# Kernel optimization log

Measured on AMD Instinct MI355X. Metric: run time of the kernel, lower is better.

## Reference

```python
import jax, jax.numpy as jnp
import numpy as np

NEG_INF = -1000000000.0


def setup_inputs() -> dict:
    key = jax.random.key(0)
    k1, k2, k3, k4, k5 = jax.random.split(key, 5)
    B, L1, L2, F1, F2, A = 64, 1024, 1024, 128, 128, 128
    feature1 = jax.random.normal(k1, (B, L1, F1), dtype=jnp.float32)
    feature2 = jax.random.normal(k2, (B, L2, F2), dtype=jnp.float32)
    mask = jax.random.randint(k3, (B, L1, L2), 0, 2, dtype=jnp.int32)
    # Linear weights stored torch-style: [out_features, in_features]
    W1 = jax.random.normal(k4, (A, F1), dtype=jnp.float32) / np.sqrt(F1)
    b1 = jnp.zeros((A,), dtype=jnp.float32)
    W2 = jax.random.normal(k5, (A, F2), dtype=jnp.float32) / np.sqrt(F2)
    b2 = jnp.zeros((A,), dtype=jnp.float32)
    return {"feature1": feature1, "feature2": feature2, "mask": mask,
            "W1": W1, "b1": b1, "W2": W2, "b2": b2}


def reference(feature1, feature2, mask, W1, b1, W2, b2):
    A = W1.shape[0]
    scale = jnp.sqrt(jnp.float32(A))
    q = jnp.einsum('bld,ad->bla', feature1, W1) + b1  # [B, L1, A]
    k = jnp.einsum('bmd,ad->bma', feature2, W2) + b2  # [B, L2, A]
    a = jnp.einsum('bla,bma->blm', q, k) / scale       # [B, L1, L2]
    masked_a = jnp.where(mask == 0, NEG_INF, a)
    alpha1 = jax.nn.softmax(masked_a, axis=2)  # softmax over L2
    alpha2 = jax.nn.softmax(masked_a, axis=1)  # softmax over L1
    out1 = jnp.einsum('blm,blf->bmf', alpha2, feature1)  # [B, L2, F1]
    out2 = jnp.einsum('blm,bmf->blf', alpha1, feature2)  # [B, L1, F2]
    return (out1, out2)
```

## Files before the change

kernel.cpp:

```cpp
#include <hip/hip_runtime.h>
#include <stdint.h>

typedef _Float16 f16;
typedef f16 f16x4 __attribute__((ext_vector_type(4)));
typedef f16 f16x8 __attribute__((ext_vector_type(8)));
typedef float f32x4 __attribute__((ext_vector_type(4)));

constexpr float SCALE = 0.08838834764831845f;

__device__ __forceinline__ void glds16(const void* g, void* l) {
  __builtin_amdgcn_global_load_lds(
      (const __attribute__((address_space(1))) void*)g,
      (__attribute__((address_space(3))) void*)l, 16, 0, 0);
}
__device__ __forceinline__ void glds4(const void* g, void* l) {
  __builtin_amdgcn_global_load_lds(
      (const __attribute__((address_space(1))) void*)g,
      (__attribute__((address_space(3))) void*)l, 4, 0, 0);
}

__global__ __launch_bounds__(256) void pack_kernel(
    const int* __restrict__ mask, uint32_t* __restrict__ bits)
{
  const int wv = blockIdx.x * 4 + (threadIdx.x >> 6);
  const int lane = threadIdx.x & 63;
#pragma unroll 2
  for (int cc = 0; cc < 4; ++cc) {
    const size_t c = (size_t)wv * 4 + cc;
    const int4* src = (const int4*)(mask + c * 2048) + lane;
    uint32_t word = 0;
#pragma unroll
    for (int it = 0; it < 8; ++it) {
      int4 v = src[it * 64];
      uint32_t nib = (v.x ? 1u : 0u) | (v.y ? 2u : 0u) |
                     (v.z ? 4u : 0u) | (v.w ? 8u : 0u);
      word |= nib << (it * 4);
    }
    bits[c * 64 + lane] = word;
  }
}

__global__ __launch_bounds__(256) void proj_kernel(
    const float* __restrict__ f1, const float* __restrict__ f2,
    const float* __restrict__ W1, const float* __restrict__ b1,
    const float* __restrict__ W2, const float* __restrict__ b2,
    f16* __restrict__ q_h, f16* __restrict__ k_h,
    f16* __restrict__ f1t, f16* __restrict__ f2t)
{
  __shared__ f16 a_lds[128 * 128];
  __shared__ f16 w_lds[128 * 128];

  const int tid = threadIdx.x;
  const int blk = blockIdx.x;
  const bool qside = blk < 512;
  const float* feat = qside ? f1 : f2;
  const float* W    = qside ? W1 : W2;
  const float* bias = qside ? b1 : b2;
  f16* op = qside ? q_h : k_h;
  f16* ft = qside ? f1t : f2t;
  const size_t row0 = (size_t)(qside ? blk : blk - 512) * 128;

  for (int it = 0; it < 16; ++it) {
    int u = tid + it * 256;
    int r = u >> 5;
    int c4 = (u & 31) * 4;
    float4 v = *(const float4*)&feat[(row0 + r) * 128 + c4];
    f16x4 h4 = { (f16)v.x, (f16)v.y, (f16)v.z, (f16)v.w };
    int adr = r * 128 + ((((c4 >> 3) ^ (r & 7)) << 3) | (c4 & 7));
    *(f16x4*)&a_lds[adr] = h4;
    float4 wv = *(const float4*)&W[r * 128 + c4];
    f16x4 wh = { (f16)wv.x, (f16)wv.y, (f16)wv.z, (f16)wv.w };
    *(f16x4*)&w_lds[adr] = wh;
  }
  __syncthreads();

  const int w = tid >> 6, l = tid & 63, lam = l & 15, g = l >> 4;
  f32x4 acc[2][8] = {};
#pragma unroll
  for (int kc = 0; kc < 4; ++kc) {
    f16x8 a[2];
#pragma unroll
    for (int rf = 0; rf < 2; ++rf) {
      int ar = w * 32 + rf * 16 + lam;
      a[rf] = *(const f16x8*)&a_lds[ar * 128 + (((4 * kc + g) ^ (ar & 7)) << 3)];
    }
#pragma unroll
    for (int cf = 0; cf < 8; ++cf) {
      int br = cf * 16 + lam;
      f16x8 bfr = *(const f16x8*)&w_lds[br * 128 + (((4 * kc + g) ^ (br & 7)) << 3)];
      acc[0][cf] = __builtin_amdgcn_mfma_f32_16x16x32_f16(a[0], bfr, acc[0][cf], 0, 0, 0);
      acc[1][cf] = __builtin_amdgcn_mfma_f32_16x16x32_f16(a[1], bfr, acc[1][cf], 0, 0, 0);
    }
  }
#pragma unroll
  for (int cf = 0; cf < 8; ++cf) {
    int col = cf * 16 + lam;
    float bv = bias[col];
#pragma unroll
    for (int rf = 0; rf < 2; ++rf)
#pragma unroll
      for (int i = 0; i < 4; ++i) {
        size_t grow = row0 + w * 32 + rf * 16 + g * 4 + i;
        op[grow * 128 + col] = (f16)(acc[rf][cf][i] + bv);
      }
  }

  {
    const int b = (int)(row0 >> 10);
    const int l0 = (int)(row0 & 1023);
    const int f = tid >> 1;
    const int half = tid & 1;
    f16 buf[64];
#pragma unroll
    for (int j = 0; j < 64; ++j) {
      int r = half * 64 + j;
      buf[j] = a_lds[r * 128 + ((((f >> 3) ^ (r & 7)) << 3) | (f & 7))];
    }
    f16* dst = ft + ((size_t)b * 128 + f) * 1024 + l0 + half * 64;
#pragma unroll
    for (int c = 0; c < 8; ++c)
      *(f16x8*)&dst[c * 8] = *(const f16x8*)&buf[c * 8];
  }
}

template <int PASS>
__global__ __launch_bounds__(256, 2) void attn_kernel(
    const f16* __restrict__ Qh, const f16* __restrict__ Kh,
    const f16* __restrict__ Vt, const uint32_t* __restrict__ bits,
    float* __restrict__ outp)
{
  __shared__ f16 k_lds[64 * 128];
  __shared__ f16 v_lds[128 * 64];
  __shared__ f16 p_lds[8 * 16 * 72];
  __shared__ uint32_t mb2[1024];

  const int tid = threadIdx.x;
  const int u = blockIdx.x;
  const int qt = (u >> 3) & 7;
  const int b = ((u >> 6) << 3) | (u & 7);
  const int w = tid >> 6, l = tid & 63, lam = l & 15, g = l >> 4;
  const size_t batch_row = (size_t)b << 10;

  f16x8 qf[2][4];
#pragma unroll
  for (int qd = 0; qd < 2; ++qd) {
    const f16* qbase = Qh + (batch_row + qt * 128 + w * 32 + qd * 16 + lam) * 128;
#pragma unroll
    for (int kc = 0; kc < 4; ++kc) qf[qd][kc] = *(const f16x8*)&qbase[kc * 32 + g * 8];
  }

  f32x4 acc[2][8] = {};
  float mrun[2][4], lrun[2][4];
#pragma unroll
  for (int qd = 0; qd < 2; ++qd)
#pragma unroll
    for (int i = 0; i < 4; ++i) { mrun[qd][i] = -__builtin_inff(); lrun[qd][i] = 0.f; }

  const f16* vtb = Vt + ((size_t)b << 17);

  for (int kt = 0; kt < 16; ++kt) {
    const int kb = kt * 64;
    __syncthreads();
    {
      const f16* kbase = Kh + (batch_row + kb) * 128;
#pragma unroll
      for (int it = 0; it < 4; ++it) {
        int slot0 = (w * 4 + it) * 64;
        int i = slot0 + l;
        int r = i >> 4, ch = i & 15;
        glds16(kbase + r * 128 + ((ch ^ (r & 7)) << 3), &k_lds[slot0 * 8]);
      }
    }
    {
#pragma unroll
      for (int it = 0; it < 4; ++it) {
        int slot0 = (w * 4 + it) * 64;
        int i = slot0 + l;
        int r = i >> 3, ch = i & 7;
        glds16(vtb + r * 1024 + kb + ((ch ^ (r & 7)) << 3), &v_lds[slot0 * 8]);
      }
    }
    {
      if constexpr (PASS == 0) {
        const uint32_t* bw = bits + ((batch_row + qt * 128) >> 1) * 64 + (kt & 3) * 16;
#pragma unroll
        for (int t = 0; t < 4; ++t) {
          int p = (w * 4 + t) * 64 + l;
          glds4(bw + (p >> 4) * 64 + ((p & 15) ^ (((p >> 4) & 3) << 2)),
                &mb2[(w * 4 + t) * 64]);
        }
      } else {
        const uint32_t* bw = bits + ((batch_row + kb) >> 1) * 64 + (qt & 1) * 32;
#pragma unroll
        for (int t = 0; t < 4; ++t) {
          int p = (w * 4 + t) * 64 + l;
          glds4(bw + (p >> 5) * 64 + ((p & 31) ^ (((p >> 5) & 7) << 2)),
                &mb2[(w * 4 + t) * 64]);
        }
      }
    }
    __syncthreads();

#pragma unroll
    for (int qd = 0; qd < 2; ++qd) {
      f32x4 sv[4] = {};
      __builtin_amdgcn_s_setprio(1);
#pragma unroll
      for (int kc = 0; kc < 4; ++kc) {
#pragma unroll
        for (int cf = 0; cf < 4; ++cf) {
          int br = cf * 16 + lam;
          f16x8 bk = *(const f16x8*)&k_lds[br * 128 + (((4 * kc + g) ^ (br & 7)) << 3)];
          sv[cf] = __builtin_amdgcn_mfma_f32_16x16x32_f16(qf[qd][kc], bk, sv[cf], 0, 0, 0);
        }
      }
      __builtin_amdgcn_s_setprio(0);

      uint32_t mk = 0;
      if constexpr (PASS == 0) {
        const int so = ((kt >> 2) << 2) + (lam & 3);
#pragma unroll
        for (int cf = 0; cf < 4; ++cf)
#pragma unroll
          for (int ih = 0; ih < 2; ++ih) {
            int rp = w * 16 + qd * 8 + g * 2 + ih;
            int s  = cf * 4 + (lam >> 2);
            uint32_t wd = mb2[rp * 16 + (s ^ ((rp & 3) << 2))];
            mk |= ((wd >> so) & 1u) << (cf * 4 + ih * 2);
            mk |= ((wd >> (16 + so)) & 1u) << (cf * 4 + ih * 2 + 1);
          }
      } else {
        const int shift = ((lam & 1) << 4) + ((qt >> 1) << 2);
        const int s1 = w * 8 + qd * 4 + g;
#pragma unroll
        for (int cf = 0; cf < 4; ++cf) {
          int rp = cf * 8 + (lam >> 1);
          uint32_t wd = mb2[rp * 32 + (s1 ^ ((rp & 7) << 2))];
          mk |= ((wd >> shift) & 15u) << (cf * 4);
        }
      }

      float mrow4[4];
#pragma unroll
      for (int i = 0; i < 4; ++i) mrow4[i] = -1e30f;
#pragma unroll
      for (int cf = 0; cf < 4; ++cf)
#pragma unroll
        for (int i = 0; i < 4; ++i) {
          float v = sv[cf][i] * SCALE;
          sv[cf][i] = v;
          mrow4[i] = fmaxf(mrow4[i], ((mk >> (cf * 4 + i)) & 1u) ? v : -1e30f);
        }
#pragma unroll
      for (int d = 1; d <= 8; d <<= 1)
#pragma unroll
        for (int i = 0; i < 4; ++i)
          mrow4[i] = fmaxf(mrow4[i], __shfl_xor(mrow4[i], d, 64));

      float sf[4], lsum[4];
#pragma unroll
      for (int i = 0; i < 4; ++i) {
        float mn = fmaxf(mrun[qd][i], mrow4[i]);
        sf[i] = __expf(mrun[qd][i] - mn);
        mrun[qd][i] = mn;
        lsum[i] = 0.f;
      }
      f16* pslice = &p_lds[(w * 2 + qd) * 1152];
#pragma unroll
      for (int cf = 0; cf < 4; ++cf)
#pragma unroll
        for (int i = 0; i < 4; ++i) {
          float p = ((mk >> (cf * 4 + i)) & 1u) ? __expf(sv[cf][i] - mrun[qd][i]) : 0.f;
          lsum[i] += p;
          int row = g * 4 + i;
          int cchunk = 2 * cf + (lam >> 3);
          pslice[row * 72 + (((cchunk ^ (row & 7)) << 3) | (lam & 7))] = (f16)p;
        }
#pragma unroll
      for (int d = 1; d <= 8; d <<= 1)
#pragma unroll
        for (int i = 0; i < 4; ++i)
          lsum[i] += __shfl_xor(lsum[i], d, 64);
#pragma unroll
      for (int i = 0; i < 4; ++i) lrun[qd][i] = lrun[qd][i] * sf[i] + lsum[i];
#pragma unroll
      for (int nf = 0; nf < 8; ++nf)
#pragma unroll
        for (int i = 0; i < 4; ++i) acc[qd][nf][i] *= sf[i];
    }

    __builtin_amdgcn_s_setprio(1);
#pragma unroll
    for (int kc2 = 0; kc2 < 2; ++kc2) {
      f16x8 ap0 = *(const f16x8*)&p_lds[(w * 2 + 0) * 1152 + lam * 72 + (((4 * kc2 + g) ^ (lam & 7)) << 3)];
      f16x8 ap1 = *(const f16x8*)&p_lds[(w * 2 + 1) * 1152 + lam * 72 + (((4 * kc2 + g) ^ (lam & 7)) << 3)];
#pragma unroll
      for (int nf = 0; nf < 8; ++nf) {
        int vr = nf * 16 + lam;
        f16x8 bv = *(const f16x8*)&v_lds[vr * 64 + (((kc2 * 4 + g) ^ (vr & 7)) << 3)];
        acc[0][nf] = __builtin_amdgcn_mfma_f32_16x16x32_f16(ap0, bv, acc[0][nf], 0, 0, 0);
        acc[1][nf] = __builtin_amdgcn_mfma_f32_16x16x32_f16(ap1, bv, acc[1][nf], 0, 0, 0);
      }
    }
    __builtin_amdgcn_s_setprio(0);
  }

#pragma unroll
  for (int qd = 0; qd < 2; ++qd) {
    float inv[4];
#pragma unroll
    for (int i = 0; i < 4; ++i) inv[i] = (lrun[qd][i] > 0.f) ? 1.f / lrun[qd][i] : 0.f;
    const size_t orow0 = batch_row + (size_t)qt * 128 + w * 32 + qd * 16;
#pragma unroll
    for (int nf = 0; nf < 8; ++nf)
#pragma unroll
      for (int i = 0; i < 4; ++i)
        outp[(orow0 + g * 4 + i) * 128 + nf * 16 + lam] = acc[qd][nf][i] * inv[i];
  }
}

extern "C" void kernel_launch(void* const* d_in, const int* in_sizes, int n_in,
                              void* d_out, int out_size, void* d_ws, size_t ws_size,
                              hipStream_t stream) {
  const float* f1 = (const float*)d_in[0];
  const float* f2 = (const float*)d_in[1];
  const int* mask = (const int*)d_in[2];
  const float* W1 = (const float*)d_in[3];
  const float* b1 = (const float*)d_in[4];
  const float* W2 = (const float*)d_in[5];
  const float* b2 = (const float*)d_in[6];
  float* out = (float*)d_out;

  if (ws_size < (size_t)3 * 8388608 * sizeof(f16) + 8388608) return;

  f16* q_h = (f16*)d_ws;
  f16* k_h = q_h + 8388608;
  f16* f1t = k_h + 8388608;
  uint32_t* bits = (uint32_t*)(f1t + 8388608);
  f16* f2t = (f16*)d_out;

  pack_kernel<<<2048, 256, 0, stream>>>(mask, bits);
  proj_kernel<<<1024, 256, 0, stream>>>(f1, f2, W1, b1, W2, b2, q_h, k_h, f1t, f2t);
  attn_kernel<0><<<512, 256, 0, stream>>>(q_h, k_h, f2t, bits, out + 8388608);
  attn_kernel<1><<<512, 256, 0, stream>>>(k_h, q_h, f1t, bits, out);
}
```

Baseline: 257.1 us.

## Fuse mask bit-packing into first attention pass and keep packed tile in LDS

```diff
diff --git a/kernel.cpp b/kernel.cpp
--- a/kernel.cpp
+++ b/kernel.cpp
@@ -17,27 +17,6 @@
   __builtin_amdgcn_global_load_lds(
       (const __attribute__((address_space(1))) void*)g,
       (__attribute__((address_space(3))) void*)l, 4, 0, 0);
-}
-
-__global__ __launch_bounds__(256) void pack_kernel(
-    const int* __restrict__ mask, uint32_t* __restrict__ bits)
-{
-  const int wv = blockIdx.x * 4 + (threadIdx.x >> 6);
-  const int lane = threadIdx.x & 63;
-#pragma unroll 2
-  for (int cc = 0; cc < 4; ++cc) {
-    const size_t c = (size_t)wv * 4 + cc;
-    const int4* src = (const int4*)(mask + c * 2048) + lane;
-    uint32_t word = 0;
-#pragma unroll
-    for (int it = 0; it < 8; ++it) {
-      int4 v = src[it * 64];
-      uint32_t nib = (v.x ? 1u : 0u) | (v.y ? 2u : 0u) |
-                     (v.z ? 4u : 0u) | (v.w ? 8u : 0u);
-      word |= nib << (it * 4);
-    }
-    bits[c * 64 + lane] = word;
-  }
 }
 
 __global__ __launch_bounds__(256) void proj_kernel(
@@ -126,13 +105,14 @@
 template <int PASS>
 __global__ __launch_bounds__(256, 2) void attn_kernel(
     const f16* __restrict__ Qh, const f16* __restrict__ Kh,
-    const f16* __restrict__ Vt, const uint32_t* __restrict__ bits,
+    const f16* __restrict__ Vt,
+    const int* __restrict__ mask, uint32_t* __restrict__ bits,
     float* __restrict__ outp)
 {
   __shared__ f16 k_lds[64 * 128];
   __shared__ f16 v_lds[128 * 64];
   __shared__ f16 p_lds[8 * 16 * 72];
-  __shared__ uint32_t mb2[1024];
+  __shared__ uint32_t mball[(PASS == 0) ? 64 * 65 : 1024];
 
   const int tid = threadIdx.x;
   const int u = blockIdx.x;
@@ -149,6 +129,24 @@
     for (int kc = 0; kc < 4; ++kc) qf[qd][kc] = *(const f16x8*)&qbase[kc * 32 + g * 8];
   }
 
+  if constexpr (PASS == 0) {
+    const int cbase = (int)(batch_row >> 1) + qt * 64;
+    for (int cc = 0; cc < 16; ++cc) {
+      const int c_local = w * 16 + cc;
+      const int4* src = (const int4*)(mask + (size_t)(cbase + c_local) * 2048) + l;
+      uint32_t word = 0;
+#pragma unroll
+      for (int it = 0; it < 8; ++it) {
+        int4 v = src[it * 64];
+        uint32_t nib = (v.x ? 1u : 0u) | (v.y ? 2u : 0u) |
+                       (v.z ? 4u : 0u) | (v.w ? 8u : 0u);
+        word |= nib << (it * 4);
+      }
+      mball[c_local * 65 + l] = word;
+      bits[(size_t)(cbase + c_local) * 64 + l] = word;
+    }
+  }
+
   f32x4 acc[2][8] = {};
   float mrun[2][4], lrun[2][4];
 #pragma unroll
@@ -180,23 +178,13 @@
         glds16(vtb + r * 1024 + kb + ((ch ^ (r & 7)) << 3), &v_lds[slot0 * 8]);
       }
     }
-    {
-      if constexpr (PASS == 0) {
-        const uint32_t* bw = bits + ((batch_row + qt * 128) >> 1) * 64 + (kt & 3) * 16;
-#pragma unroll
-        for (int t = 0; t < 4; ++t) {
-          int p = (w * 4 + t) * 64 + l;
-          glds4(bw + (p >> 4) * 64 + ((p & 15) ^ (((p >> 4) & 3) << 2)),
-                &mb2[(w * 4 + t) * 64]);
-        }
-      } else {
-        const uint32_t* bw = bits + ((batch_row + kb) >> 1) * 64 + (qt & 1) * 32;
-#pragma unroll
-        for (int t = 0; t < 4; ++t) {
-          int p = (w * 4 + t) * 64 + l;
-          glds4(bw + (p >> 5) * 64 + ((p & 31) ^ (((p >> 5) & 7) << 2)),
-                &mb2[(w * 4 + t) * 64]);
-        }
+    if constexpr (PASS == 1) {
+      const uint32_t* bw = bits + ((batch_row + kb) >> 1) * 64 + (qt & 1) * 32;
+#pragma unroll
+      for (int t = 0; t < 4; ++t) {
+        int p = (w * 4 + t) * 64 + l;
+        glds4(bw + (p >> 5) * 64 + ((p & 31) ^ (((p >> 5) & 7) << 2)),
+              &mball[(w * 4 + t) * 64]);
       }
     }
     __syncthreads();
@@ -224,8 +212,8 @@
 #pragma unroll
           for (int ih = 0; ih < 2; ++ih) {
             int rp = w * 16 + qd * 8 + g * 2 + ih;
-            int s  = cf * 4 + (lam >> 2);
-            uint32_t wd = mb2[rp * 16 + (s ^ ((rp & 3) << 2))];
+            int sp = (kt & 3) * 16 + cf * 4 + (lam >> 2);
+            uint32_t wd = mball[rp * 65 + sp];
             mk |= ((wd >> so) & 1u) << (cf * 4 + ih * 2);
             mk |= ((wd >> (16 + so)) & 1u) << (cf * 4 + ih * 2 + 1);
           }
@@ -235,7 +223,7 @@
 #pragma unroll
         for (int cf = 0; cf < 4; ++cf) {
           int rp = cf * 8 + (lam >> 1);
-          uint32_t wd = mb2[rp * 32 + (s1 ^ ((rp & 7) << 2))];
+          uint32_t wd = mball[rp * 32 + (s1 ^ ((rp & 7) << 2))];
           mk |= ((wd >> shift) & 15u) << (cf * 4);
         }
       }
@@ -339,8 +327,9 @@
   uint32_t* bits = (uint32_t*)(f1t + 8388608);
   f16* f2t = (f16*)d_out;
 
-  pack_kernel<<<2048, 256, 0, stream>>>(mask, bits);
   proj_kernel<<<1024, 256, 0, stream>>>(f1, f2, W1, b1, W2, b2, q_h, k_h, f1t, f2t);
-  attn_kernel<0><<<512, 256, 0, stream>>>(q_h, k_h, f2t, bits, out + 8388608);
-  attn_kernel<1><<<512, 256, 0, stream>>>(k_h, q_h, f1t, bits, out);
-}
+  attn_kernel<0><<<512, 256, 0, stream>>>(q_h, k_h, f2t, mask, bits,
+                                          out + 8388608);
+  attn_kernel<1><<<512, 256, 0, stream>>>(k_h, q_h, f1t, nullptr, bits,
+                                          out);
+}
```

New measurement: 260.9 us. Within noise of the previous version (+1.5%).
